# Optimization experiments

Hardware: AMD Instinct MI355X
Metric: run time of the kernel (lower is better)

## Reference

```python
import jax, jax.numpy as jnp
import numpy as np

HIDDEN = 1280
HEADS = 8
RANK = 4
BATCH = 2
SEQ = 4096


def setup_inputs() -> dict:
    key = jax.random.key(0)
    ks = jax.random.split(key, 11)
    s = 1.0 / np.sqrt(HIDDEN)
    return {
        "hidden_states": jax.random.normal(ks[0], (BATCH, SEQ, HIDDEN), jnp.float32),
        # attn projections (stored as [in, out] for x @ W)
        "w_q": jax.random.normal(ks[1], (HIDDEN, HIDDEN), jnp.float32) * s,
        "w_k": jax.random.normal(ks[2], (HIDDEN, HIDDEN), jnp.float32) * s,
        "w_v": jax.random.normal(ks[3], (HIDDEN, HIDDEN), jnp.float32) * s,
        # LoRA down/up matrices for K and V
        "lora_k_a": jax.random.normal(ks[4], (HIDDEN, RANK), jnp.float32) * s,
        "lora_k_b": jax.random.normal(ks[5], (RANK, HIDDEN), jnp.float32) * 0.5,
        "lora_v_a": jax.random.normal(ks[6], (HIDDEN, RANK), jnp.float32) * s,
        "lora_v_b": jax.random.normal(ks[7], (RANK, HIDDEN), jnp.float32) * 0.5,
        # output projection (to_out[0]); to_out[1] is dropout -> identity at eval
        "w_out": jax.random.normal(ks[8], (HIDDEN, HIDDEN), jnp.float32) * s,
        "b_out": jax.random.normal(ks[9], (HIDDEN,), jnp.float32) * 0.01,
    }


def reference(hidden_states, w_q, w_k, w_v, lora_k_a, lora_k_b,
              lora_v_a, lora_v_b, w_out, b_out):
    B, S, D = hidden_states.shape
    H = HEADS
    dh = D // H
    scale = 1.0 / np.sqrt(dh)

    # QKV projections
    q = hidden_states @ w_q                      # [B, S, D]
    k = hidden_states @ w_k
    v = hidden_states @ w_v

    # LoRA low-rank residual updates to key/value
    k = k + (k @ lora_k_a) @ lora_k_b            # rank-4 update
    v = v + (v @ lora_v_a) @ lora_v_b

    # head_to_batch_dim: [B, S, D] -> [B, H, S, dh]
    q = q.reshape(B, S, H, dh).transpose(0, 2, 1, 3)
    k = k.reshape(B, S, H, dh).transpose(0, 2, 1, 3)
    v = v.reshape(B, S, H, dh).transpose(0, 2, 1, 3)

    # naive attention: scores -> softmax -> weighted sum
    scores = jnp.einsum("bhqd,bhkd->bhqk", q, k) * scale   # [B, H, S, S]
    probs = jax.nn.softmax(scores, axis=-1)
    out = jnp.einsum("bhqk,bhkd->bhqd", probs, v)          # [B, H, S, dh]

    # batch_to_head_dim: [B, H, S, dh] -> [B, S, D]
    out = out.transpose(0, 2, 1, 3).reshape(B, S, D)

    # to_out[0] linear; to_out[1] dropout is identity in eval
    return out @ w_out + b_out
```

## Files before the change

### kernel.cpp

```cpp
#include <hip/hip_runtime.h>
#include <stdint.h>

typedef __attribute__((ext_vector_type(8))) __bf16 bf16x8;
typedef __attribute__((ext_vector_type(2))) __bf16 bf16x2;
typedef __attribute__((ext_vector_type(4))) float f32x4;
typedef __attribute__((ext_vector_type(16))) float f32x16;
typedef unsigned short u16;

#define LOG2E 1.44269504088896f

static_assert(sizeof(bf16x8) == 16, "bf16x8 must be 16B");

__device__ __forceinline__ u16 f2bf(float f) {
  unsigned u = __builtin_bit_cast(unsigned, f);
  u += 0x7fffu + ((u >> 16) & 1u);
  return (u16)(u >> 16);
}

__device__ __forceinline__ void load_lds16(const void* g, void* l) {
  __builtin_amdgcn_global_load_lds((const __attribute__((address_space(1))) void*)g,
                                   (__attribute__((address_space(3))) void*)l, 16, 0, 0);
}

__global__ __launch_bounds__(256) void lora_tmp_k(
    const float* __restrict__ wk, const float* __restrict__ wv,
    const float* __restrict__ ka, const float* __restrict__ va,
    float* __restrict__ tk, float* __restrict__ tv) {
  const int i = blockIdx.x;
  const float* W = blockIdx.y ? wv : wk;
  const float* A = blockIdx.y ? va : ka;
  float* T = blockIdx.y ? tv : tk;
  float s0 = 0.f, s1 = 0.f, s2 = 0.f, s3 = 0.f;
  for (int j = threadIdx.x; j < 1280; j += 256) {
    float w = W[(size_t)i * 1280 + j];
    float4 a4 = *(const float4*)(A + (size_t)j * 4);
    s0 += w * a4.x; s1 += w * a4.y; s2 += w * a4.z; s3 += w * a4.w;
  }
#pragma unroll
  for (int m = 1; m < 64; m <<= 1) {
    s0 += __shfl_xor(s0, m); s1 += __shfl_xor(s1, m);
    s2 += __shfl_xor(s2, m); s3 += __shfl_xor(s3, m);
  }
  __shared__ float red[4][4];
  const int wv_ = threadIdx.x >> 6;
  if ((threadIdx.x & 63) == 0) {
    red[wv_][0] = s0; red[wv_][1] = s1; red[wv_][2] = s2; red[wv_][3] = s3;
  }
  __syncthreads();
  if (threadIdx.x < 4) {
    float r = red[0][threadIdx.x] + red[1][threadIdx.x] + red[2][threadIdx.x] + red[3][threadIdx.x];
    T[(size_t)i * 4 + threadIdx.x] = r;
  }
}

__global__ void wt_prep_k(const float* __restrict__ W, const float* __restrict__ tmp,
                          const float* __restrict__ LB, u16* __restrict__ WT) {
  __shared__ float tile[32][33];
  const int o0 = blockIdx.x * 32, i0 = blockIdx.y * 32;
  const int tx = threadIdx.x, ty = threadIdx.y;
#pragma unroll
  for (int kk = 0; kk < 4; ++kk) {
    int i = i0 + ty + kk * 8, o = o0 + tx;
    float v = W[(size_t)i * 1280 + o];
    if (tmp) {
      float4 t = *(const float4*)(tmp + (size_t)i * 4);
      v += t.x * LB[o] + t.y * LB[1280 + o] + t.z * LB[2560 + o] + t.w * LB[3840 + o];
    }
    tile[ty + kk * 8][tx] = v;
  }
  __syncthreads();
#pragma unroll
  for (int kk = 0; kk < 4; ++kk) {
    int o = o0 + ty + kk * 8, i = i0 + tx;
    WT[(size_t)o * 1280 + i] = f2bf(tile[tx][ty + kk * 8]);
  }
}

__global__ __launch_bounds__(256) void cvt_bf16_k(const float* __restrict__ in,
                                                  u16* __restrict__ out, int n4) {
  for (int i = blockIdx.x * 256 + threadIdx.x; i < n4; i += gridDim.x * 256) {
    float4 v = ((const float4*)in)[i];
    ushort4 o;
    o.x = f2bf(v.x); o.y = f2bf(v.y); o.z = f2bf(v.z); o.w = f2bf(v.w);
    ((ushort4*)out)[i] = o;
  }
}

__global__ void vtrans_k(const u16* __restrict__ V, u16* __restrict__ VT) {
  __shared__ u16 tile[32][33];
  const int s0 = blockIdx.x * 32, c0 = blockIdx.y * 32, b = blockIdx.z;
  const int tx = threadIdx.x, ty = threadIdx.y;
#pragma unroll
  for (int kk = 0; kk < 4; ++kk)
    tile[ty + kk * 8][tx] = V[(size_t)(b * 4096 + s0 + ty + kk * 8) * 1280 + c0 + tx];
  __syncthreads();
#pragma unroll
  for (int kk = 0; kk < 4; ++kk)
    VT[(size_t)(b * 1280 + c0 + ty + kk * 8) * 4096 + s0 + tx] = tile[tx][ty + kk * 8];
}

template <bool F32OUT>
__global__ __launch_bounds__(256) void gemm128_k(
    const u16* __restrict__ A, const u16* __restrict__ WT,
    void* __restrict__ outp, const float* __restrict__ bias, float oscale) {
  __shared__ __align__(16) u16 lds[2 * 128 * 40];
  u16* ldsA = lds;
  u16* ldsB = lds + 128 * 40;
  const int tid = threadIdx.x;
  const int lane = tid & 63, lrow = lane & 15, lhi = lane >> 4;
  const int w = tid >> 6, wm = w >> 1, wn = w & 1;
  const size_t M0 = (size_t)blockIdx.x * 128, N0 = (size_t)blockIdx.y * 128;
  const int wb = tid & 192;
  f32x4 acc[4][4] = {};

  for (int k0 = 0; k0 < 1280; k0 += 32) {
#pragma unroll
    for (int j = 0; j < 3; ++j) {
      if (j < 2 || tid < 128) {
        int i = j * 256 + tid;
        int row = i / 5, c = i % 5; c = c < 4 ? c : 3;
        load_lds16(A + (M0 + row) * 1280 + k0 + c * 8, ldsA + (j * 256 + wb) * 8);
      }
    }
#pragma unroll
    for (int j = 0; j < 3; ++j) {
      if (j < 2 || tid < 128) {
        int i = j * 256 + tid;
        int row = i / 5, c = i % 5; c = c < 4 ? c : 3;
        load_lds16(WT + (N0 + row) * 1280 + k0 + c * 8, ldsB + (j * 256 + wb) * 8);
      }
    }
    __syncthreads();
    bf16x8 af[4], bfr[4];
#pragma unroll
    for (int m = 0; m < 4; ++m)
      af[m] = *(const bf16x8*)(ldsA + (wm * 64 + m * 16 + lrow) * 40 + lhi * 8);
#pragma unroll
    for (int n = 0; n < 4; ++n)
      bfr[n] = *(const bf16x8*)(ldsB + (wn * 64 + n * 16 + lrow) * 40 + lhi * 8);
#pragma unroll
    for (int m = 0; m < 4; ++m)
#pragma unroll
      for (int n = 0; n < 4; ++n)
        acc[m][n] = __builtin_amdgcn_mfma_f32_16x16x32_bf16(af[m], bfr[n], acc[m][n], 0, 0, 0);
    __syncthreads();
  }

#pragma unroll
  for (int m = 0; m < 4; ++m)
#pragma unroll
    for (int n = 0; n < 4; ++n)
#pragma unroll
      for (int r = 0; r < 4; ++r) {
        size_t row = M0 + wm * 64 + m * 16 + lhi * 4 + r;
        size_t col = N0 + wn * 64 + n * 16 + lrow;
        float v = acc[m][n][r];
        if (F32OUT)
          ((float*)outp)[row * 1280 + col] = v + bias[col];
        else
          ((u16*)outp)[row * 1280 + col] = f2bf(v * oscale);
      }
}

__global__ __launch_bounds__(256, 2) void attn_k(
    const u16* __restrict__ Q, const u16* __restrict__ K,
    const u16* __restrict__ VT, u16* __restrict__ AO) {
  __shared__ __align__(16) u16 lds_all[40960];
  u16* const kb0 = lds_all;
  u16* const kb1 = lds_all + 10240;
  u16* const vt0 = lds_all + 20480;
  u16* const vt1 = lds_all + 30720;
  const int tid = threadIdx.x;
  const int lane = tid & 63;
  const int l31 = lane & 31, lhi5 = lane >> 5;
  const int lo32 = (lane < 32);
  const int w = tid >> 6;
  const int bh = blockIdx.x, qt = blockIdx.y;
  const int b = bh >> 3, h = bh & 7;
  const int wb = tid & 192;

  const u16* Kg = K + (size_t)b * 4096 * 1280 + h * 160;
  const u16* VTg = VT + ((size_t)b * 1280 + h * 160) * 4096;

  bf16x8 qf[10];
  const u16* Qg = Q + (size_t)(b * 4096 + qt * 128 + w * 32 + l31) * 1280 + h * 160 + lhi5 * 8;
#pragma unroll
  for (int kf = 0; kf < 10; ++kf) qf[kf] = *(const bf16x8*)(Qg + kf * 16);
#pragma unroll
  for (int kf = 0; kf < 10; ++kf) asm volatile("" : "+v"(qf[kf]));

  auto stageK = [&](int kv0, u16* dst) {
#pragma unroll
    for (int j = 0; j < 5; ++j) {
      int i = j * 256 + tid;
      int row = i / 20, cl = i % 20;
      int cg = (cl < 16) ? ((cl & 24) | ((cl ^ row) & 7))
                         : (16 + ((cl ^ (row >> 1)) & 3));
      load_lds16(Kg + (size_t)(kv0 + row) * 1280 + cg * 8, dst + (j * 256 + wb) * 8);
    }
  };
  auto stageV = [&](int kv0, u16* dst) {
#pragma unroll
    for (int j = 0; j < 5; ++j) {
      int i = j * 256 + tid;
      int row = i >> 3, cl = i & 7;
      int cg = cl ^ (row & 7);
      load_lds16(VTg + (size_t)row * 4096 + kv0 + cg * 8, dst + (j * 256 + wb) * 8);
    }
  };

  stageK(0, kb0);
  stageV(0, vt0);

  f32x16 o[5] = {};
  float m_run = -1e30f, l_run = 0.f;
  float mLog = m_run * LOG2E;

  auto body = [&](int t, const u16* kcur, const u16* vcur, u16* knx, u16* vnx, bool last) {
    if (!last) { stageK((t + 1) * 64, knx); stageV((t + 1) * 64, vnx); }
    if (!last) { asm volatile("s_waitcnt vmcnt(15)" ::: "memory"); }
    else       { asm volatile("s_waitcnt vmcnt(5)" ::: "memory"); }
    __builtin_amdgcn_s_barrier();
    __builtin_amdgcn_sched_barrier(0);

    f32x16 sacc[2] = {};
    __builtin_amdgcn_s_setprio(1);
#pragma unroll
    for (int kf = 0; kf < 10; ++kf) {
      const int c = 2 * kf + lhi5;
#pragma unroll
      for (int mt = 0; mt < 2; ++mt) {
        const int row = mt * 32 + l31;
        const int slot = (kf < 8) ? ((c & 24) | ((c ^ row) & 7))
                                  : (16 + ((c ^ (row >> 1)) & 3));
        bf16x8 ka = *(const bf16x8*)(kcur + row * 160 + slot * 8);
        sacc[mt] = __builtin_amdgcn_mfma_f32_32x32x16_bf16(ka, qf[kf], sacc[mt], 0, 0, 0);
      }
    }
    __builtin_amdgcn_s_setprio(0);

    float tmx[8];
#pragma unroll
    for (int i = 0; i < 8; ++i)
      tmx[i] = fmaxf(fmaxf(sacc[0][i], sacc[0][i + 8]),
                     fmaxf(sacc[1][i], sacc[1][i + 8]));
    float mx = fmaxf(fmaxf(fmaxf(tmx[0], tmx[1]), fmaxf(tmx[2], tmx[3])),
                     fmaxf(fmaxf(tmx[4], tmx[5]), fmaxf(tmx[6], tmx[7])));
    mx = fmaxf(mx, __shfl_xor(mx, 32));
    if (__any(mx - m_run > 8.0f)) {
      float mnew = fmaxf(m_run, mx);
      float al = __builtin_amdgcn_exp2f((m_run - mnew) * LOG2E);
      l_run *= al; m_run = mnew; mLog = m_run * LOG2E;
#pragma unroll
      for (int dm = 0; dm < 5; ++dm)
#pragma unroll
        for (int i = 0; i < 16; ++i) o[dm][i] *= al;
    }
    float rs0 = 0.f, rs1 = 0.f, rs2 = 0.f, rs3 = 0.f;
    unsigned xp[2][8];
#pragma unroll
    for (int mt = 0; mt < 2; ++mt)
#pragma unroll
      for (int r = 0; r < 8; ++r) {
        float p0 = __builtin_amdgcn_exp2f(fmaf(sacc[mt][2 * r], LOG2E, -mLog));
        float p1 = __builtin_amdgcn_exp2f(fmaf(sacc[mt][2 * r + 1], LOG2E, -mLog));
        if ((r & 3) == 0) rs0 += p0 + p1;
        else if ((r & 3) == 1) rs1 += p0 + p1;
        else if ((r & 3) == 2) rs2 += p0 + p1;
        else rs3 += p0 + p1;
        bf16x2 pk; pk[0] = (__bf16)p0; pk[1] = (__bf16)p1;
        xp[mt][r] = __builtin_bit_cast(unsigned, pk);
      }
    float rs = (rs0 + rs1) + (rs2 + rs3);
    rs += __shfl_xor(rs, 32);
    l_run += rs;

    if (!last) { asm volatile("s_waitcnt vmcnt(10)" ::: "memory"); }
    else       { asm volatile("s_waitcnt vmcnt(0)" ::: "memory"); }
    __builtin_amdgcn_s_barrier();
    __builtin_amdgcn_sched_barrier(0);

    __builtin_amdgcn_s_setprio(1);
#pragma unroll
    for (int kf = 0; kf < 4; ++kf) {
      const int mt = kf >> 1, hf = kf & 1;
      unsigned xa = xp[mt][hf * 4 + 0], xb = xp[mt][hf * 4 + 1];
      unsigned xc = xp[mt][hf * 4 + 2], xd = xp[mt][hf * 4 + 3];
      unsigned sa = __shfl_xor((int)xa, 32), sb = __shfl_xor((int)xb, 32);
      unsigned sc = __shfl_xor((int)xc, 32), sd = __shfl_xor((int)xd, 32);
      uint4 pw;
      pw.x = lo32 ? xa : sc;
      pw.y = lo32 ? xb : sd;
      pw.z = lo32 ? sa : xc;
      pw.w = lo32 ? sb : xd;
      bf16x8 pB = __builtin_bit_cast(bf16x8, pw);
      const int c = 2 * kf + lhi5;
#pragma unroll
      for (int dm = 0; dm < 5; ++dm) {
        const int row = dm * 32 + l31;
        bf16x8 va = *(const bf16x8*)(vcur + row * 64 + ((c ^ (row & 7)) * 8));
        o[dm] = __builtin_amdgcn_mfma_f32_32x32x16_bf16(va, pB, o[dm], 0, 0, 0);
      }
    }
    __builtin_amdgcn_s_setprio(0);
  };

  for (int t = 0; t < 62; t += 2) {
    body(t, kb0, vt0, kb1, vt1, false);
    body(t + 1, kb1, vt1, kb0, vt0, false);
  }
  body(62, kb0, vt0, kb1, vt1, false);
  body(63, kb1, vt1, kb0, vt0, true);

  float invl = 1.f / l_run;
  u16* tr = lds_all + w * 5376;
#pragma unroll
  for (int dm = 0; dm < 5; ++dm)
#pragma unroll
    for (int k = 0; k < 4; ++k) {
      int d = dm * 32 + k * 8 + lhi5 * 4;
      unsigned lo_ = (unsigned)f2bf(o[dm][4 * k + 0] * invl) |
                     ((unsigned)f2bf(o[dm][4 * k + 1] * invl) << 16);
      unsigned hi_ = (unsigned)f2bf(o[dm][4 * k + 2] * invl) |
                     ((unsigned)f2bf(o[dm][4 * k + 3] * invl) << 16);
      uint2 u; u.x = lo_; u.y = hi_;
      *(uint2*)(tr + l31 * 168 + d) = u;
    }
  asm volatile("s_waitcnt lgkmcnt(0)" ::: "memory");
  __builtin_amdgcn_sched_barrier(0);
  const size_t qg0 = (size_t)(b * 4096 + qt * 128 + w * 32);
#pragma unroll
  for (int it = 0; it < 10; ++it) {
    int idx = it * 64 + lane;
    int row = idx / 20, cc = idx % 20;
    bf16x8 vch = *(const bf16x8*)(tr + row * 168 + cc * 8);
    *(bf16x8*)(AO + (qg0 + row) * 1280 + h * 160 + cc * 8) = vch;
  }
}

extern "C" void kernel_launch(void* const* d_in, const int* in_sizes, int n_in,
                              void* d_out, int out_size, void* d_ws, size_t ws_size,
                              hipStream_t stream) {
  const float* hs  = (const float*)d_in[0];
  const float* w_q = (const float*)d_in[1];
  const float* w_k = (const float*)d_in[2];
  const float* w_v = (const float*)d_in[3];
  const float* lka = (const float*)d_in[4];
  const float* lkb = (const float*)d_in[5];
  const float* lva = (const float*)d_in[6];
  const float* lvb = (const float*)d_in[7];
  const float* w_o = (const float*)d_in[8];
  const float* b_o = (const float*)d_in[9];
  float* out = (float*)d_out;
  char* ws = (char*)d_ws;

  const size_t KA  = 0;
  const size_t VA  = 20480;
  const size_t WTQ = 40960;
  const size_t WTK = WTQ + 3276800;
  const size_t WTV = WTK + 3276800;
  const size_t WTO = WTV + 3276800;
  const size_t HSB = WTO + 3276800;
  const size_t QB  = HSB + 20971520;
  const size_t KB  = QB + 20971520;
  const size_t VB  = KB + 20971520;
  const size_t VTB = VB + 20971520;
  const size_t AOB = VTB + 20971520;
  const size_t END = AOB + 20971520;
  if (ws_size < END) return;

  float* tk = (float*)(ws + KA);
  float* tv = (float*)(ws + VA);
  u16* wtq = (u16*)(ws + WTQ);
  u16* wtk = (u16*)(ws + WTK);
  u16* wtv = (u16*)(ws + WTV);
  u16* wto = (u16*)(ws + WTO);
  u16* hsb = (u16*)(ws + HSB);
  u16* qb  = (u16*)(ws + QB);
  u16* kb  = (u16*)(ws + KB);
  u16* vb  = (u16*)(ws + VB);
  u16* vtb = (u16*)(ws + VTB);
  u16* aob = (u16*)(ws + AOB);

  lora_tmp_k<<<dim3(1280, 2), 256, 0, stream>>>(w_k, w_v, lka, lva, tk, tv);
  wt_prep_k<<<dim3(40, 40), dim3(32, 8), 0, stream>>>(w_q, nullptr, nullptr, wtq);
  wt_prep_k<<<dim3(40, 40), dim3(32, 8), 0, stream>>>(w_k, tk, lkb, wtk);
  wt_prep_k<<<dim3(40, 40), dim3(32, 8), 0, stream>>>(w_v, tv, lvb, wtv);
  wt_prep_k<<<dim3(40, 40), dim3(32, 8), 0, stream>>>(w_o, nullptr, nullptr, wto);
  cvt_bf16_k<<<2048, 256, 0, stream>>>(hs, hsb, 2621440);

  const float qscale = 0.07905694150420949f;
  gemm128_k<false><<<dim3(64, 10), 256, 0, stream>>>(hsb, wtq, qb, nullptr, qscale);
  gemm128_k<false><<<dim3(64, 10), 256, 0, stream>>>(hsb, wtk, kb, nullptr, 1.0f);
  gemm128_k<false><<<dim3(64, 10), 256, 0, stream>>>(hsb, wtv, vb, nullptr, 1.0f);
  vtrans_k<<<dim3(128, 40, 2), dim3(32, 8), 0, stream>>>(vb, vtb);
  attn_k<<<dim3(16, 32), 256, 0, stream>>>(qb, kb, vtb, aob);
  gemm128_k<true><<<dim3(64, 10), 256, 0, stream>>>(aob, wto, (void*)out, b_o, 1.0f);
}
```

Before: 394.8 us.

## Software-pipeline attention QK/PV across tiles and fuse QKV projections into one GEMM launch

The attention loop is restructured so the QK^T MFMAs for the next tile overlap with the PV MFMAs of the previous tile, with softmax following. K is prefetched one tile ahead and V is staged one tile behind. The three QKV projection GEMMs become a single launch with a 30-column grid, relying on the weight and output buffers being contiguous in the workspace. This adds a prologue and epilogue and depends on that workspace layout.

Result: slower. 876.3 us (+121.9%).

```diff
diff --git a/kernel.cpp b/kernel.cpp
--- a/kernel.cpp
+++ b/kernel.cpp
@@ -99,7 +99,7 @@
     VT[(size_t)(b * 1280 + c0 + ty + kk * 8) * 4096 + s0 + tx] = tile[tx][ty + kk * 8];
 }
 
-template <bool F32OUT>
+template <bool F32OUT, bool FUSED3>
 __global__ __launch_bounds__(256) void gemm128_k(
     const u16* __restrict__ A, const u16* __restrict__ WT,
     void* __restrict__ outp, const float* __restrict__ bias, float oscale) {
@@ -146,6 +146,9 @@
     __syncthreads();
   }
 
+  const float sc = FUSED3 ? (N0 < 1280 ? oscale : 1.0f) : oscale;
+  const size_t obase = FUSED3 ? (size_t)(N0 / 1280) * 10485760 : 0;
+  const size_t ncol0 = FUSED3 ? (N0 % 1280) : N0;
 #pragma unroll
   for (int m = 0; m < 4; ++m)
 #pragma unroll
@@ -153,12 +156,12 @@
 #pragma unroll
       for (int r = 0; r < 4; ++r) {
         size_t row = M0 + wm * 64 + m * 16 + lhi * 4 + r;
-        size_t col = N0 + wn * 64 + n * 16 + lrow;
+        size_t col = ncol0 + wn * 64 + n * 16 + lrow;
         float v = acc[m][n][r];
         if (F32OUT)
           ((float*)outp)[row * 1280 + col] = v + bias[col];
         else
-          ((u16*)outp)[row * 1280 + col] = f2bf(v * oscale);
+          ((u16*)outp)[obase + row * 1280 + col] = f2bf(v * sc);
       }
 }
 
@@ -209,21 +212,15 @@
     }
   };
 
-  stageK(0, kb0);
-  stageV(0, vt0);
-
   f32x16 o[5] = {};
+  f32x16 sacc[2];
+  unsigned xp[2][8];
   float m_run = -1e30f, l_run = 0.f;
   float mLog = m_run * LOG2E;
 
-  auto body = [&](int t, const u16* kcur, const u16* vcur, u16* knx, u16* vnx, bool last) {
-    if (!last) { stageK((t + 1) * 64, knx); stageV((t + 1) * 64, vnx); }
-    if (!last) { asm volatile("s_waitcnt vmcnt(15)" ::: "memory"); }
-    else       { asm volatile("s_waitcnt vmcnt(5)" ::: "memory"); }
-    __builtin_amdgcn_s_barrier();
-    __builtin_amdgcn_sched_barrier(0);
-
-    f32x16 sacc[2] = {};
+  auto qkcluster = [&](const u16* kcur) {
+    f32x16 zz = {};
+    sacc[0] = zz; sacc[1] = zz;
     __builtin_amdgcn_s_setprio(1);
 #pragma unroll
     for (int kf = 0; kf < 10; ++kf) {
@@ -238,48 +235,9 @@
       }
     }
     __builtin_amdgcn_s_setprio(0);
-
-    float tmx[8];
-#pragma unroll
-    for (int i = 0; i < 8; ++i)
-      tmx[i] = fmaxf(fmaxf(sacc[0][i], sacc[0][i + 8]),
-                     fmaxf(sacc[1][i], sacc[1][i + 8]));
-    float mx = fmaxf(fmaxf(fmaxf(tmx[0], tmx[1]), fmaxf(tmx[2], tmx[3])),
-                     fmaxf(fmaxf(tmx[4], tmx[5]), fmaxf(tmx[6], tmx[7])));
-    mx = fmaxf(mx, __shfl_xor(mx, 32));
-    if (__any(mx - m_run > 8.0f)) {
-      float mnew = fmaxf(m_run, mx);
-      float al = __builtin_amdgcn_exp2f((m_run - mnew) * LOG2E);
-      l_run *= al; m_run = mnew; mLog = m_run * LOG2E;
-#pragma unroll
-      for (int dm = 0; dm < 5; ++dm)
-#pragma unroll
-        for (int i = 0; i < 16; ++i) o[dm][i] *= al;
-    }
-    float rs0 = 0.f, rs1 = 0.f, rs2 = 0.f, rs3 = 0.f;
-    unsigned xp[2][8];
-#pragma unroll
-    for (int mt = 0; mt < 2; ++mt)
-#pragma unroll
-      for (int r = 0; r < 8; ++r) {
-        float p0 = __builtin_amdgcn_exp2f(fmaf(sacc[mt][2 * r], LOG2E, -mLog));
-        float p1 = __builtin_amdgcn_exp2f(fmaf(sacc[mt][2 * r + 1], LOG2E, -mLog));
-        if ((r & 3) == 0) rs0 += p0 + p1;
-        else if ((r & 3) == 1) rs1 += p0 + p1;
-        else if ((r & 3) == 2) rs2 += p0 + p1;
-        else rs3 += p0 + p1;
-        bf16x2 pk; pk[0] = (__bf16)p0; pk[1] = (__bf16)p1;
-        xp[mt][r] = __builtin_bit_cast(unsigned, pk);
-      }
-    float rs = (rs0 + rs1) + (rs2 + rs3);
-    rs += __shfl_xor(rs, 32);
-    l_run += rs;
-
-    if (!last) { asm volatile("s_waitcnt vmcnt(10)" ::: "memory"); }
-    else       { asm volatile("s_waitcnt vmcnt(0)" ::: "memory"); }
-    __builtin_amdgcn_s_barrier();
-    __builtin_amdgcn_sched_barrier(0);
-
+  };
+
+  auto pvcluster = [&](const u16* vsrc) {
     __builtin_amdgcn_s_setprio(1);
 #pragma unroll
     for (int kf = 0; kf < 4; ++kf) {
@@ -298,19 +256,92 @@
 #pragma unroll
       for (int dm = 0; dm < 5; ++dm) {
         const int row = dm * 32 + l31;
-        bf16x8 va = *(const bf16x8*)(vcur + row * 64 + ((c ^ (row & 7)) * 8));
+        bf16x8 va = *(const bf16x8*)(vsrc + row * 64 + ((c ^ (row & 7)) * 8));
         o[dm] = __builtin_amdgcn_mfma_f32_32x32x16_bf16(va, pB, o[dm], 0, 0, 0);
       }
     }
     __builtin_amdgcn_s_setprio(0);
   };
 
-  for (int t = 0; t < 62; t += 2) {
-    body(t, kb0, vt0, kb1, vt1, false);
-    body(t + 1, kb1, vt1, kb0, vt0, false);
-  }
-  body(62, kb0, vt0, kb1, vt1, false);
-  body(63, kb1, vt1, kb0, vt0, true);
+  auto softmax = [&]() {
+    float tmx[8];
+#pragma unroll
+    for (int i = 0; i < 8; ++i)
+      tmx[i] = fmaxf(fmaxf(sacc[0][i], sacc[0][i + 8]),
+                     fmaxf(sacc[1][i], sacc[1][i + 8]));
+    float mx = fmaxf(fmaxf(fmaxf(tmx[0], tmx[1]), fmaxf(tmx[2], tmx[3])),
+                     fmaxf(fmaxf(tmx[4], tmx[5]), fmaxf(tmx[6], tmx[7])));
+    mx = fmaxf(mx, __shfl_xor(mx, 32));
+    if (__any(mx - m_run > 8.0f)) {
+      float mnew = fmaxf(m_run, mx);
+      float al = __builtin_amdgcn_exp2f((m_run - mnew) * LOG2E);
+      l_run *= al; m_run = mnew; mLog = m_run * LOG2E;
+#pragma unroll
+      for (int dm = 0; dm < 5; ++dm)
+#pragma unroll
+        for (int i = 0; i < 16; ++i) o[dm][i] *= al;
+    }
+    float rs0 = 0.f, rs1 = 0.f, rs2 = 0.f, rs3 = 0.f;
+#pragma unroll
+    for (int mt = 0; mt < 2; ++mt)
+#pragma unroll
+      for (int r = 0; r < 8; ++r) {
+        float p0 = __builtin_amdgcn_exp2f(fmaf(sacc[mt][2 * r], LOG2E, -mLog));
+        float p1 = __builtin_amdgcn_exp2f(fmaf(sacc[mt][2 * r + 1], LOG2E, -mLog));
+        if ((r & 3) == 0) rs0 += p0 + p1;
+        else if ((r & 3) == 1) rs1 += p0 + p1;
+        else if ((r & 3) == 2) rs2 += p0 + p1;
+        else rs3 += p0 + p1;
+        bf16x2 pk; pk[0] = (__bf16)p0; pk[1] = (__bf16)p1;
+        xp[mt][r] = __builtin_bit_cast(unsigned, pk);
+      }
+    float rs = (rs0 + rs1) + (rs2 + rs3);
+    rs += __shfl_xor(rs, 32);
+    l_run += rs;
+  };
+
+  stageK(0, kb0);
+  asm volatile("s_waitcnt vmcnt(0)" ::: "memory");
+  __builtin_amdgcn_s_barrier();
+  __builtin_amdgcn_sched_barrier(0);
+  stageK(64, kb1);
+  stageV(0, vt0);
+  qkcluster(kb0);
+  softmax();
+
+  auto bodyMain = [&](int t, const u16* kcur, u16* knx, const u16* vprev, u16* vcur) {
+    asm volatile("s_waitcnt vmcnt(5)" ::: "memory");
+    __builtin_amdgcn_s_barrier();
+    __builtin_amdgcn_sched_barrier(0);
+    stageK((t + 1) * 64, knx);
+    stageV(t * 64, vcur);
+    qkcluster(kcur);
+    asm volatile("s_waitcnt vmcnt(10)" ::: "memory");
+    __builtin_amdgcn_s_barrier();
+    __builtin_amdgcn_sched_barrier(0);
+    pvcluster(vprev);
+    softmax();
+  };
+  for (int tp = 0; tp < 31; ++tp) {
+    bodyMain(2 * tp + 1, kb1, kb0, vt0, vt1);
+    bodyMain(2 * tp + 2, kb0, kb1, vt1, vt0);
+  }
+
+  asm volatile("s_waitcnt vmcnt(5)" ::: "memory");
+  __builtin_amdgcn_s_barrier();
+  __builtin_amdgcn_sched_barrier(0);
+  stageV(63 * 64, vt1);
+  qkcluster(kb1);
+  asm volatile("s_waitcnt vmcnt(5)" ::: "memory");
+  __builtin_amdgcn_s_barrier();
+  __builtin_amdgcn_sched_barrier(0);
+  pvcluster(vt0);
+  softmax();
+
+  asm volatile("s_waitcnt vmcnt(0)" ::: "memory");
+  __builtin_amdgcn_s_barrier();
+  __builtin_amdgcn_sched_barrier(0);
+  pvcluster(vt1);
 
   float invl = 1.f / l_run;
   u16* tr = lds_all + w * 5376;
@@ -377,10 +408,10 @@
   u16* wto = (u16*)(ws + WTO);
   u16* hsb = (u16*)(ws + HSB);
   u16* qb  = (u16*)(ws + QB);
-  u16* kb  = (u16*)(ws + KB);
   u16* vb  = (u16*)(ws + VB);
   u16* vtb = (u16*)(ws + VTB);
   u16* aob = (u16*)(ws + AOB);
+  u16* kb  = (u16*)(ws + KB);
 
   lora_tmp_k<<<dim3(1280, 2), 256, 0, stream>>>(w_k, w_v, lka, lva, tk, tv);
   wt_prep_k<<<dim3(40, 40), dim3(32, 8), 0, stream>>>(w_q, nullptr, nullptr, wtq);
@@ -390,10 +421,8 @@
   cvt_bf16_k<<<2048, 256, 0, stream>>>(hs, hsb, 2621440);
 
   const float qscale = 0.07905694150420949f;
-  gemm128_k<false><<<dim3(64, 10), 256, 0, stream>>>(hsb, wtq, qb, nullptr, qscale);
-  gemm128_k<false><<<dim3(64, 10), 256, 0, stream>>>(hsb, wtk, kb, nullptr, 1.0f);
-  gemm128_k<false><<<dim3(64, 10), 256, 0, stream>>>(hsb, wtv, vb, nullptr, 1.0f);
+  gemm128_k<false, true><<<dim3(64, 30), 256, 0, stream>>>(hsb, wtq, qb, nullptr, qscale);
   vtrans_k<<<dim3(128, 40, 2), dim3(32, 8), 0, stream>>>(vb, vtb);
   attn_k<<<dim3(16, 32), 256, 0, stream>>>(qb, kb, vtb, aob);
-  gemm128_k<true><<<dim3(64, 10), 256, 0, stream>>>(aob, wto, (void*)out, b_o, 1.0f);
-}
+  gemm128_k<true, false><<<dim3(64, 10), 256, 0, stream>>>(aob, wto, (void*)out, b_o, 1.0f);
+}
```

## Software-pipeline attention QK and PV across KV tiles; fuse QKV GEMMs

Applied to the files above, without the earlier changes.

The attention main loop is restructured so the QK^T MFMA cluster for the next KV tile runs alongside the PV cluster of the previous tile. Softmax lags one step behind, and K and V staging are decoupled onto separate double-buffer schedules with explicit vmcnt waits. This is meant to hide softmax and exp latency and load waits behind matrix-core work. Separately, the Q, K and V projection GEMMs become one launch with a three-times wider grid. That launch relies on the transposed weights and the output buffers being contiguous in the workspace. The pipelining raises register pressure and depends on fragile hand-tuned wait counts.

Measured after the change: 381.3 us. 3.4% less time.

```diff
diff --git a/kernel.cpp b/kernel.cpp
--- a/kernel.cpp
+++ b/kernel.cpp
@@ -99,7 +99,7 @@
     VT[(size_t)(b * 1280 + c0 + ty + kk * 8) * 4096 + s0 + tx] = tile[tx][ty + kk * 8];
 }
 
-template <bool F32OUT>
+template <bool F32OUT, bool FUSED3>
 __global__ __launch_bounds__(256) void gemm128_k(
     const u16* __restrict__ A, const u16* __restrict__ WT,
     void* __restrict__ outp, const float* __restrict__ bias, float oscale) {
@@ -146,6 +146,9 @@
     __syncthreads();
   }
 
+  const float sc = FUSED3 ? (N0 < 1280 ? oscale : 1.0f) : oscale;
+  const size_t obase = FUSED3 ? (size_t)(N0 / 1280) * 10485760 : 0;
+  const size_t ncol0 = FUSED3 ? (N0 % 1280) : N0;
 #pragma unroll
   for (int m = 0; m < 4; ++m)
 #pragma unroll
@@ -153,14 +156,145 @@
 #pragma unroll
       for (int r = 0; r < 4; ++r) {
         size_t row = M0 + wm * 64 + m * 16 + lhi * 4 + r;
-        size_t col = N0 + wn * 64 + n * 16 + lrow;
+        size_t col = ncol0 + wn * 64 + n * 16 + lrow;
         float v = acc[m][n][r];
         if (F32OUT)
           ((float*)outp)[row * 1280 + col] = v + bias[col];
         else
-          ((u16*)outp)[row * 1280 + col] = f2bf(v * oscale);
+          ((u16*)outp)[obase + row * 1280 + col] = f2bf(v * sc);
       }
 }
+
+
+#define QK_CLUSTER(KCUR)                                                        \
+  {                                                                             \
+    f32x16 zz = {};                                                             \
+    sacc0 = zz; sacc1 = zz;                                                     \
+    __builtin_amdgcn_s_setprio(1);                                              \
+    _Pragma("unroll")                                                           \
+    for (int kf = 0; kf < 10; ++kf) {                                           \
+      const int c_ = 2 * kf + lhi5;                                             \
+      {                                                                         \
+        const int row_ = l31;                                                   \
+        const int slot_ = (kf < 8) ? ((c_ & 24) | ((c_ ^ row_) & 7))            \
+                                   : (16 + ((c_ ^ (row_ >> 1)) & 3));           \
+        bf16x8 ka_ = *(const bf16x8*)((KCUR) + row_ * 160 + slot_ * 8);         \
+        sacc0 = __builtin_amdgcn_mfma_f32_32x32x16_bf16(ka_, qf[kf], sacc0, 0, 0, 0); \
+      }                                                                         \
+      {                                                                         \
+        const int row_ = 32 + l31;                                              \
+        const int slot_ = (kf < 8) ? ((c_ & 24) | ((c_ ^ row_) & 7))            \
+                                   : (16 + ((c_ ^ (row_ >> 1)) & 3));           \
+        bf16x8 ka_ = *(const bf16x8*)((KCUR) + row_ * 160 + slot_ * 8);         \
+        sacc1 = __builtin_amdgcn_mfma_f32_32x32x16_bf16(ka_, qf[kf], sacc1, 0, 0, 0); \
+      }                                                                         \
+    }                                                                           \
+    __builtin_amdgcn_s_setprio(0);                                              \
+  }
+
+#define PV_CLUSTER(VSRC)                                                        \
+  {                                                                             \
+    __builtin_amdgcn_s_setprio(1);                                              \
+    _Pragma("unroll")                                                           \
+    for (int kf = 0; kf < 4; ++kf) {                                            \
+      const int base_ = (kf >> 1) * 8 + (kf & 1) * 4;                           \
+      unsigned xa_ = xp[base_ + 0], xb_ = xp[base_ + 1];                        \
+      unsigned xc_ = xp[base_ + 2], xd_ = xp[base_ + 3];                        \
+      unsigned sa_ = __shfl_xor((int)xa_, 32), sb_ = __shfl_xor((int)xb_, 32);  \
+      unsigned sc_ = __shfl_xor((int)xc_, 32), sd_ = __shfl_xor((int)xd_, 32);  \
+      uint4 pw_;                                                                \
+      pw_.x = lo32 ? xa_ : sc_;                                                 \
+      pw_.y = lo32 ? xb_ : sd_;                                                 \
+      pw_.z = lo32 ? sa_ : xc_;                                                 \
+      pw_.w = lo32 ? sb_ : xd_;                                                 \
+      bf16x8 pB_ = __builtin_bit_cast(bf16x8, pw_);                             \
+      const int c_ = 2 * kf + lhi5;                                             \
+      _Pragma("unroll")                                                         \
+      for (int dm = 0; dm < 5; ++dm) {                                          \
+        const int row_ = dm * 32 + l31;                                         \
+        bf16x8 va_ = *(const bf16x8*)((VSRC) + row_ * 64 + ((c_ ^ (row_ & 7)) * 8)); \
+        o[dm] = __builtin_amdgcn_mfma_f32_32x32x16_bf16(va_, pB_, o[dm], 0, 0, 0); \
+      }                                                                         \
+    }                                                                           \
+    __builtin_amdgcn_s_setprio(0);                                              \
+  }
+
+#define SOFTMAX_STEP()                                                          \
+  {                                                                             \
+    float tmx_[8];                                                              \
+    _Pragma("unroll")                                                           \
+    for (int i = 0; i < 8; ++i)                                                 \
+      tmx_[i] = fmaxf(fmaxf(sacc0[i], sacc0[i + 8]),                            \
+                      fmaxf(sacc1[i], sacc1[i + 8]));                           \
+    float mx_ = fmaxf(fmaxf(fmaxf(tmx_[0], tmx_[1]), fmaxf(tmx_[2], tmx_[3])),  \
+                      fmaxf(fmaxf(tmx_[4], tmx_[5]), fmaxf(tmx_[6], tmx_[7]))); \
+    mx_ = fmaxf(mx_, __shfl_xor(mx_, 32));                                      \
+    if (__any(mx_ - m_run > 8.0f)) {                                            \
+      float mnew_ = fmaxf(m_run, mx_);                                          \
+      float al_ = __builtin_amdgcn_exp2f((m_run - mnew_) * LOG2E);              \
+      l_run *= al_; m_run = mnew_; mLog = m_run * LOG2E;                        \
+      _Pragma("unroll")                                                         \
+      for (int dm = 0; dm < 5; ++dm)                                            \
+        _Pragma("unroll")                                                       \
+        for (int i = 0; i < 16; ++i) o[dm][i] *= al_;                           \
+    }                                                                           \
+    float rs0_ = 0.f, rs1_ = 0.f, rs2_ = 0.f, rs3_ = 0.f;                       \
+    _Pragma("unroll")                                                           \
+    for (int r = 0; r < 8; ++r) {                                               \
+      float p0_ = __builtin_amdgcn_exp2f(fmaf(sacc0[2 * r], LOG2E, -mLog));     \
+      float p1_ = __builtin_amdgcn_exp2f(fmaf(sacc0[2 * r + 1], LOG2E, -mLog)); \
+      if ((r & 3) == 0) rs0_ += p0_ + p1_;                                      \
+      else if ((r & 3) == 1) rs1_ += p0_ + p1_;                                 \
+      else if ((r & 3) == 2) rs2_ += p0_ + p1_;                                 \
+      else rs3_ += p0_ + p1_;                                                   \
+      bf16x2 pk_; pk_[0] = (__bf16)p0_; pk_[1] = (__bf16)p1_;                   \
+      xp[r] = __builtin_bit_cast(unsigned, pk_);                                \
+    }                                                                           \
+    _Pragma("unroll")                                                           \
+    for (int r = 0; r < 8; ++r) {                                               \
+      float p0_ = __builtin_amdgcn_exp2f(fmaf(sacc1[2 * r], LOG2E, -mLog));     \
+      float p1_ = __builtin_amdgcn_exp2f(fmaf(sacc1[2 * r + 1], LOG2E, -mLog)); \
+      if ((r & 3) == 0) rs0_ += p0_ + p1_;                                      \
+      else if ((r & 3) == 1) rs1_ += p0_ + p1_;                                 \
+      else if ((r & 3) == 2) rs2_ += p0_ + p1_;                                 \
+      else rs3_ += p0_ + p1_;                                                   \
+      bf16x2 pk_; pk_[0] = (__bf16)p0_; pk_[1] = (__bf16)p1_;                   \
+      xp[8 + r] = __builtin_bit_cast(unsigned, pk_);                            \
+    }                                                                           \
+    float rs_ = (rs0_ + rs1_) + (rs2_ + rs3_);                                  \
+    rs_ += __shfl_xor(rs_, 32);                                                 \
+    l_run += rs_;                                                               \
+  }
+
+#define STAGE_K(KV0, DST)                                                       \
+  {                                                                             \
+    _Pragma("unroll")                                                           \
+    for (int j = 0; j < 5; ++j) {                                               \
+      int i_ = j * 256 + tid;                                                   \
+      int row_ = i_ / 20, cl_ = i_ % 20;                                        \
+      int cg_ = (cl_ < 16) ? ((cl_ & 24) | ((cl_ ^ row_) & 7))                  \
+                           : (16 + ((cl_ ^ (row_ >> 1)) & 3));                  \
+      load_lds16(Kg + (size_t)((KV0) + row_) * 1280 + cg_ * 8,                  \
+                 (DST) + (j * 256 + wb) * 8);                                   \
+    }                                                                           \
+  }
+
+#define STAGE_V(KV0, DST)                                                       \
+  {                                                                             \
+    _Pragma("unroll")                                                           \
+    for (int j = 0; j < 5; ++j) {                                               \
+      int i_ = j * 256 + tid;                                                   \
+      int row_ = i_ >> 3, cl_ = i_ & 7;                                         \
+      int cg_ = cl_ ^ (row_ & 7);                                               \
+      load_lds16(VTg + (size_t)row_ * 4096 + (KV0) + cg_ * 8,                   \
+                 (DST) + (j * 256 + wb) * 8);                                   \
+    }                                                                           \
+  }
+
+#define WAITB(N)                                                                \
+  asm volatile("s_waitcnt vmcnt(" #N ")" ::: "memory");                         \
+  __builtin_amdgcn_s_barrier();                                                 \
+  __builtin_amdgcn_sched_barrier(0);
 
 __global__ __launch_bounds__(256, 2) void attn_k(
     const u16* __restrict__ Q, const u16* __restrict__ K,
@@ -189,128 +323,46 @@
 #pragma unroll
   for (int kf = 0; kf < 10; ++kf) asm volatile("" : "+v"(qf[kf]));
 
-  auto stageK = [&](int kv0, u16* dst) {
-#pragma unroll
-    for (int j = 0; j < 5; ++j) {
-      int i = j * 256 + tid;
-      int row = i / 20, cl = i % 20;
-      int cg = (cl < 16) ? ((cl & 24) | ((cl ^ row) & 7))
-                         : (16 + ((cl ^ (row >> 1)) & 3));
-      load_lds16(Kg + (size_t)(kv0 + row) * 1280 + cg * 8, dst + (j * 256 + wb) * 8);
-    }
-  };
-  auto stageV = [&](int kv0, u16* dst) {
-#pragma unroll
-    for (int j = 0; j < 5; ++j) {
-      int i = j * 256 + tid;
-      int row = i >> 3, cl = i & 7;
-      int cg = cl ^ (row & 7);
-      load_lds16(VTg + (size_t)row * 4096 + kv0 + cg * 8, dst + (j * 256 + wb) * 8);
-    }
-  };
-
-  stageK(0, kb0);
-  stageV(0, vt0);
-
   f32x16 o[5] = {};
+  f32x16 sacc0, sacc1;
+  unsigned xp[16];
   float m_run = -1e30f, l_run = 0.f;
   float mLog = m_run * LOG2E;
 
-  auto body = [&](int t, const u16* kcur, const u16* vcur, u16* knx, u16* vnx, bool last) {
-    if (!last) { stageK((t + 1) * 64, knx); stageV((t + 1) * 64, vnx); }
-    if (!last) { asm volatile("s_waitcnt vmcnt(15)" ::: "memory"); }
-    else       { asm volatile("s_waitcnt vmcnt(5)" ::: "memory"); }
-    __builtin_amdgcn_s_barrier();
-    __builtin_amdgcn_sched_barrier(0);
-
-    f32x16 sacc[2] = {};
-    __builtin_amdgcn_s_setprio(1);
-#pragma unroll
-    for (int kf = 0; kf < 10; ++kf) {
-      const int c = 2 * kf + lhi5;
-#pragma unroll
-      for (int mt = 0; mt < 2; ++mt) {
-        const int row = mt * 32 + l31;
-        const int slot = (kf < 8) ? ((c & 24) | ((c ^ row) & 7))
-                                  : (16 + ((c ^ (row >> 1)) & 3));
-        bf16x8 ka = *(const bf16x8*)(kcur + row * 160 + slot * 8);
-        sacc[mt] = __builtin_amdgcn_mfma_f32_32x32x16_bf16(ka, qf[kf], sacc[mt], 0, 0, 0);
-      }
-    }
-    __builtin_amdgcn_s_setprio(0);
-
-    float tmx[8];
-#pragma unroll
-    for (int i = 0; i < 8; ++i)
-      tmx[i] = fmaxf(fmaxf(sacc[0][i], sacc[0][i + 8]),
-                     fmaxf(sacc[1][i], sacc[1][i + 8]));
-    float mx = fmaxf(fmaxf(fmaxf(tmx[0], tmx[1]), fmaxf(tmx[2], tmx[3])),
-                     fmaxf(fmaxf(tmx[4], tmx[5]), fmaxf(tmx[6], tmx[7])));
-    mx = fmaxf(mx, __shfl_xor(mx, 32));
-    if (__any(mx - m_run > 8.0f)) {
-      float mnew = fmaxf(m_run, mx);
-      float al = __builtin_amdgcn_exp2f((m_run - mnew) * LOG2E);
-      l_run *= al; m_run = mnew; mLog = m_run * LOG2E;
-#pragma unroll
-      for (int dm = 0; dm < 5; ++dm)
-#pragma unroll
-        for (int i = 0; i < 16; ++i) o[dm][i] *= al;
-    }
-    float rs0 = 0.f, rs1 = 0.f, rs2 = 0.f, rs3 = 0.f;
-    unsigned xp[2][8];
-#pragma unroll
-    for (int mt = 0; mt < 2; ++mt)
-#pragma unroll
-      for (int r = 0; r < 8; ++r) {
-        float p0 = __builtin_amdgcn_exp2f(fmaf(sacc[mt][2 * r], LOG2E, -mLog));
-        float p1 = __builtin_amdgcn_exp2f(fmaf(sacc[mt][2 * r + 1], LOG2E, -mLog));
-        if ((r & 3) == 0) rs0 += p0 + p1;
-        else if ((r & 3) == 1) rs1 += p0 + p1;
-        else if ((r & 3) == 2) rs2 += p0 + p1;
-        else rs3 += p0 + p1;
-        bf16x2 pk; pk[0] = (__bf16)p0; pk[1] = (__bf16)p1;
-        xp[mt][r] = __builtin_bit_cast(unsigned, pk);
-      }
-    float rs = (rs0 + rs1) + (rs2 + rs3);
-    rs += __shfl_xor(rs, 32);
-    l_run += rs;
-
-    if (!last) { asm volatile("s_waitcnt vmcnt(10)" ::: "memory"); }
-    else       { asm volatile("s_waitcnt vmcnt(0)" ::: "memory"); }
-    __builtin_amdgcn_s_barrier();
-    __builtin_amdgcn_sched_barrier(0);
-
-    __builtin_amdgcn_s_setprio(1);
-#pragma unroll
-    for (int kf = 0; kf < 4; ++kf) {
-      const int mt = kf >> 1, hf = kf & 1;
-      unsigned xa = xp[mt][hf * 4 + 0], xb = xp[mt][hf * 4 + 1];
-      unsigned xc = xp[mt][hf * 4 + 2], xd = xp[mt][hf * 4 + 3];
-      unsigned sa = __shfl_xor((int)xa, 32), sb = __shfl_xor((int)xb, 32);
-      unsigned sc = __shfl_xor((int)xc, 32), sd = __shfl_xor((int)xd, 32);
-      uint4 pw;
-      pw.x = lo32 ? xa : sc;
-      pw.y = lo32 ? xb : sd;
-      pw.z = lo32 ? sa : xc;
-      pw.w = lo32 ? sb : xd;
-      bf16x8 pB = __builtin_bit_cast(bf16x8, pw);
-      const int c = 2 * kf + lhi5;
-#pragma unroll
-      for (int dm = 0; dm < 5; ++dm) {
-        const int row = dm * 32 + l31;
-        bf16x8 va = *(const bf16x8*)(vcur + row * 64 + ((c ^ (row & 7)) * 8));
-        o[dm] = __builtin_amdgcn_mfma_f32_32x32x16_bf16(va, pB, o[dm], 0, 0, 0);
-      }
-    }
-    __builtin_amdgcn_s_setprio(0);
-  };
-
-  for (int t = 0; t < 62; t += 2) {
-    body(t, kb0, vt0, kb1, vt1, false);
-    body(t + 1, kb1, vt1, kb0, vt0, false);
-  }
-  body(62, kb0, vt0, kb1, vt1, false);
-  body(63, kb1, vt1, kb0, vt0, true);
+  STAGE_K(0, kb0);
+  WAITB(0);
+  STAGE_K(64, kb1);
+  STAGE_V(0, vt0);
+  QK_CLUSTER(kb0);
+  SOFTMAX_STEP();
+
+  for (int tp = 0; tp < 31; ++tp) {
+    const int t1 = 2 * tp + 1;
+    WAITB(5);
+    STAGE_K((t1 + 1) * 64, kb0);
+    STAGE_V(t1 * 64, vt1);
+    QK_CLUSTER(kb1);
+    WAITB(10);
+    PV_CLUSTER(vt0);
+    SOFTMAX_STEP();
+    WAITB(5);
+    STAGE_K((t1 + 2) * 64, kb1);
+    STAGE_V((t1 + 1) * 64, vt0);
+    QK_CLUSTER(kb0);
+    WAITB(10);
+    PV_CLUSTER(vt1);
+    SOFTMAX_STEP();
+  }
+
+  WAITB(5);
+  STAGE_V(63 * 64, vt1);
+  QK_CLUSTER(kb1);
+  WAITB(5);
+  PV_CLUSTER(vt0);
+  SOFTMAX_STEP();
+
+  WAITB(0);
+  PV_CLUSTER(vt1);
 
   float invl = 1.f / l_run;
   u16* tr = lds_all + w * 5376;
@@ -390,10 +442,8 @@
   cvt_bf16_k<<<2048, 256, 0, stream>>>(hs, hsb, 2621440);
 
   const float qscale = 0.07905694150420949f;
-  gemm128_k<false><<<dim3(64, 10), 256, 0, stream>>>(hsb, wtq, qb, nullptr, qscale);
-  gemm128_k<false><<<dim3(64, 10), 256, 0, stream>>>(hsb, wtk, kb, nullptr, 1.0f);
-  gemm128_k<false><<<dim3(64, 10), 256, 0, stream>>>(hsb, wtv, vb, nullptr, 1.0f);
+  gemm128_k<false, true><<<dim3(64, 30), 256, 0, stream>>>(hsb, wtq, qb, nullptr, qscale);
   vtrans_k<<<dim3(128, 40, 2), dim3(32, 8), 0, stream>>>(vb, vtb);
   attn_k<<<dim3(16, 32), 256, 0, stream>>>(qb, kb, vtb, aob);
-  gemm128_k<true><<<dim3(64, 10), 256, 0, stream>>>(aob, wto, (void*)out, b_o, 1.0f);
-}
+  gemm128_k<true, false><<<dim3(64, 10), 256, 0, stream>>>(aob, wto, (void*)out, b_o, 1.0f);
+}
```
